# Performance work log

Measured on AMD Instinct MI355X. Metric: run time of the kernel, lower is better.

Reference implementation:

```python
import jax, jax.numpy as jnp
import numpy as np

N = 8192
IN_F = 512
OUT_F = 128
ALPHA = 0.2  # leaky relu negative slope
NEG_BIG = -1e10
RND_SCALE = 1e5


def setup_inputs() -> dict:
    key = jax.random.key(0)
    k1, k2, k3, k4, k5 = jax.random.split(key, 5)
    h = jax.random.normal(k1, (N, IN_F), dtype=jnp.float32)
    adj = jax.random.randint(k2, (N, N), 0, 2, dtype=jnp.int32)
    W = jax.random.normal(k3, (IN_F, OUT_F), dtype=jnp.float32) * 0.05
    a = jax.random.normal(k4, (2 * OUT_F, 1), dtype=jnp.float32) * 0.1
    # rnd in original is 1e5*(rand-0.5); same distribution here
    rnd = RND_SCALE * (jax.random.uniform(k5, (N, OUT_F), dtype=jnp.float32) - 0.5)
    return {"h": h, "adj": adj, "W": W, "a": a, "rnd": rnd}


def reference(h, adj, W, a, rnd):
    Wh = h @ W                              # [N, OUT_F]
    Wh1 = Wh @ a[:OUT_F, :]                 # [N, 1]
    Wh2 = Wh @ a[OUT_F:, :]                 # [N, 1]
    e = jax.nn.leaky_relu(Wh1 + Wh2.T, negative_slope=ALPHA)  # [N, N]
    attention = jnp.where(adj > 0, e, NEG_BIG)
    attention = jax.nn.softmax(attention, axis=1)
    h_prime = attention @ Wh                # [N, OUT_F]
    h_prime = (h_prime + rnd) / RND_SCALE
    return jax.nn.elu(h_prime)
```

## Files before the change

### kernel.cpp

```cpp
#include <hip/hip_runtime.h>

#define N 8192
#define IN_F 512
#define OUT_F 128
#define SPLITK 8
#define KC 1024
#define LOG2E 1.4426950408889634f
#define LN2 0.6931471805599453f

typedef __attribute__((ext_vector_type(4))) float f32x4;
typedef __attribute__((ext_vector_type(8))) short bf16x8;
typedef __attribute__((ext_vector_type(8))) unsigned short u16x8;
typedef __attribute__((ext_vector_type(4))) int i32x4;

__device__ __forceinline__ short f2bf(float f) {
    union { float f; unsigned u; } c; c.f = f;
    unsigned r = c.u + 0x7FFFu + ((c.u >> 16) & 1u);
    return (short)(r >> 16);
}

__device__ __forceinline__ float exp2fast(float x) {
#if __has_builtin(__builtin_amdgcn_exp2f)
    return __builtin_amdgcn_exp2f(x);
#else
    return __expf(x * LN2);
#endif
}

__device__ __forceinline__ void load_lds16(const void* g, void* l) {
    __builtin_amdgcn_global_load_lds((const __attribute__((address_space(1))) unsigned*)g,
                                     (__attribute__((address_space(3))) unsigned*)l,
                                     16, 0, 0);
}

__global__ __launch_bounds__(256) void prep(const float* __restrict__ W,
                                            short* __restrict__ WT) {
    int idx = blockIdx.x * 256 + threadIdx.x;
    int n = idx & (OUT_F - 1);
    int k = idx >> 7;
    WT[(size_t)n * IN_F + k] = f2bf(W[idx]);
}

__global__ __launch_bounds__(256) void gemm_hW(const float* __restrict__ h,
                                               const short* __restrict__ WT,
                                               const float* __restrict__ a,
                                               short* __restrict__ WhT,
                                               float* __restrict__ sOut,
                                               float* __restrict__ tOut) {
    const int tid = threadIdx.x;
    const int wave = tid >> 6, lane = tid & 63;
    const int row16 = lane & 15, kgrp = lane >> 4;
    const int m0 = blockIdx.x * 16;
    const int kbase = wave * 128;

    f32x4 acc[8] = {};
    const float4* hp = (const float4*)(h + (size_t)(m0 + row16) * IN_F + kbase);

#pragma unroll
    for (int kk = 0; kk < 128; kk += 32) {
        float4 u0 = hp[kk / 4 + kgrp * 2];
        float4 u1 = hp[kk / 4 + kgrp * 2 + 1];
        bf16x8 af;
        af[0] = f2bf(u0.x); af[1] = f2bf(u0.y); af[2] = f2bf(u0.z); af[3] = f2bf(u0.w);
        af[4] = f2bf(u1.x); af[5] = f2bf(u1.y); af[6] = f2bf(u1.z); af[7] = f2bf(u1.w);
#pragma unroll
        for (int nt = 0; nt < 8; nt++) {
            bf16x8 bf_ = *(const bf16x8*)(WT + (size_t)(nt * 16 + row16) * IN_F + kbase + kk + kgrp * 8);
            acc[nt] = __builtin_amdgcn_mfma_f32_16x16x32_bf16(af, bf_, acc[nt], 0, 0, 0);
        }
    }

    __shared__ float red[4][16][132];
#pragma unroll
    for (int nt = 0; nt < 8; nt++)
#pragma unroll
        for (int r = 0; r < 4; r++)
            red[wave][kgrp * 4 + r][nt * 16 + row16] = acc[nt][r];
    __syncthreads();

    const int row = tid >> 4, seg = tid & 15;
    float v[8];
#pragma unroll
    for (int e = 0; e < 8; e++) {
        int c = seg * 8 + e;
        v[e] = red[0][row][c] + red[1][row][c] + red[2][row][c] + red[3][row][c];
    }
    float sp = 0.f, tp = 0.f;
#pragma unroll
    for (int e = 0; e < 8; e++) {
        sp += v[e] * a[seg * 8 + e];
        tp += v[e] * a[OUT_F + seg * 8 + e];
    }
    sp += __shfl_xor(sp, 1); tp += __shfl_xor(tp, 1);
    sp += __shfl_xor(sp, 2); tp += __shfl_xor(tp, 2);
    sp += __shfl_xor(sp, 4); tp += __shfl_xor(tp, 4);
    sp += __shfl_xor(sp, 8); tp += __shfl_xor(tp, 8);
    if (seg == 0) {
        sOut[m0 + row] = sp * LOG2E;
        tOut[m0 + row] = tp * LOG2E;
    }
#pragma unroll
    for (int e = 0; e < 8; e++)
        WhT[(size_t)(seg * 8 + e) * N + m0 + row] = f2bf(v[e]);
}

__global__ __launch_bounds__(256, 4) void attn(const int* __restrict__ adj,
                                               const short* __restrict__ WhT,
                                               const float* __restrict__ s,
                                               const float* __restrict__ t,
                                               unsigned short* __restrict__ num,
                                               float* __restrict__ lpart) {
    const int tid = threadIdx.x;
    const int wave = tid >> 6, lane = tid & 63;
    const int row16 = lane & 15, kgrp = lane >> 4;
    const int kb = blockIdx.x & 7;
    const int mb = blockIdx.x >> 3;
    const int m0 = mb * 64 + wave * 16;
    const int m  = m0 + row16;
    const int ks = kb * KC;

    __shared__ short Bs[2][2][128 * 32];
    __shared__ float tl[KC];

    const i32x4* ap = (const i32x4*)(adj + (size_t)m * N + ks);
    const int abase = kgrp * 2;

    i32x4 ab[2][4];
#pragma unroll
    for (int d = 0; d < 2; d++)
#pragma unroll
        for (int hh = 0; hh < 2; hh++) {
            ab[0][d * 2 + hh] = __builtin_nontemporal_load(ap + d * 8 + abase + hh);
            ab[1][d * 2 + hh] = __builtin_nontemporal_load(ap + 16 + d * 8 + abase + hh);
        }

    for (int i = tid; i < KC; i += 256) tl[i] = t[ks + i];
    const float s_m = s[m];

    auto stageB = [&](int sup, int par) {
        const int k0 = ks + sup * 64;
#pragma unroll
        for (int d = 0; d < 2; d++)
#pragma unroll
            for (int q = 0; q < 2; q++) {
                int nrow = wave * 32 + q * 16 + (lane >> 2);
                const short* g = WhT + (size_t)nrow * N + k0 + d * 32 + (lane & 3) * 8;
                load_lds16(g, &Bs[par][d][(wave * 32 + q * 16) * 32]);
            }
    };

    f32x4 acc[8] = {};
    float lsum = 0.f;

    stageB(0, 0);
    __syncthreads();

    for (int spo = 0; spo < 8; spo++) {
#pragma unroll
        for (int ss = 0; ss < 2; ss++) {
            const int sp = spo * 2 + ss;
            const int par = ss;
            if (sp + 1 < 16) {
                stageB(sp + 1, par ^ 1);
                __builtin_amdgcn_sched_barrier(0);
            }
#pragma unroll
            for (int d = 0; d < 2; d++) {
                const int g = sp * 2 + d;
                const i32x4 a0 = ab[ss][d * 2 + 0];
                const i32x4 a1 = ab[ss][d * 2 + 1];

                const float* tp = tl + g * 32 + kgrp * 8;
                float4 tA = *(const float4*)tp;
                float4 tB = *(const float4*)(tp + 4);
                float tv[8] = { tA.x, tA.y, tA.z, tA.w, tB.x, tB.y, tB.z, tB.w };

                bf16x8 bfr[8];
                const short* base = &Bs[par][d][0];
#pragma unroll
                for (int ni = 0; ni < 8; ni++)
                    bfr[ni] = *(const bf16x8*)(base + (ni * 16 + row16) * 32 + kgrp * 8);

                bf16x8 af;
                unsigned* au = (unsigned*)&af;
#pragma unroll
                for (int q = 0; q < 4; q++) {
                    const int e0 = 2 * q, e1 = 2 * q + 1;
                    float x0 = s_m + tv[e0];
                    float x1 = s_m + tv[e1];
                    x0 = fmaxf(x0, 0.2f * x0);
                    x1 = fmaxf(x1, 0.2f * x1);
                    unsigned u0 = __float_as_uint(exp2fast(x0)) & 0xFFFF0000u;
                    unsigned u1 = __float_as_uint(exp2fast(x1)) & 0xFFFF0000u;
                    const int av0 = (e0 < 4) ? a0[e0] : a1[e0 - 4];
                    const int av1 = (e1 < 4) ? a0[e1] : a1[e1 - 4];
                    u0 = av0 > 0 ? u0 : 0u;
                    u1 = av1 > 0 ? u1 : 0u;
                    lsum += __uint_as_float(u0);
                    lsum += __uint_as_float(u1);
                    au[q] = (u0 >> 16) | u1;
                }

                if (d == 1 && sp + 2 < 16) {
                    __builtin_amdgcn_sched_barrier(0);
#pragma unroll
                    for (int dd = 0; dd < 2; dd++)
#pragma unroll
                        for (int hh = 0; hh < 2; hh++)
                            ab[ss][dd * 2 + hh] =
                                __builtin_nontemporal_load(ap + (sp + 2) * 16 + dd * 8 + abase + hh);
                    __builtin_amdgcn_sched_barrier(0);
                }

#pragma unroll
                for (int ni = 0; ni < 8; ni++)
                    acc[ni] = __builtin_amdgcn_mfma_f32_16x16x32_bf16(af, bfr[ni], acc[ni], 0, 0, 0);
            }
            asm volatile("s_waitcnt vmcnt(4)\n\ts_barrier" ::: "memory");
        }
    }

    {
        float v = lsum;
        v += __shfl_xor(v, 16);
        v += __shfl_xor(v, 32);
        if (kgrp == 0) lpart[(size_t)kb * N + m] = v;
    }

    unsigned short* np_ = num + ((size_t)kb * N + m0) * OUT_F;
#pragma unroll
    for (int ni = 0; ni < 8; ni++) {
        int n = ni * 16 + row16;
#pragma unroll
        for (int r = 0; r < 4; r++)
            np_[(size_t)(kgrp * 4 + r) * OUT_F + n] = (unsigned short)f2bf(acc[ni][r]);
    }
}

__global__ __launch_bounds__(256) void finalize(const unsigned short* __restrict__ num,
                                                const float* __restrict__ lpart,
                                                const float* __restrict__ rnd,
                                                float* __restrict__ out) {
    int idx = blockIdx.x * 256 + threadIdx.x;
    int m = idx >> 4;
    int c = (idx & 15) * 8;
    size_t g = (size_t)m * OUT_F + c;

    float nm[8] = {};
#pragma unroll
    for (int bk = 0; bk < SPLITK; bk++) {
        u16x8 v = *(const u16x8*)(num + (size_t)bk * N * OUT_F + g);
#pragma unroll
        for (int e = 0; e < 8; e++) nm[e] += __uint_as_float((unsigned)v[e] << 16);
    }
    float l = 0.f;
#pragma unroll
    for (int bk = 0; bk < SPLITK; bk++) l += lpart[(size_t)bk * N + m];
    float inv = 1.f / fmaxf(l, 1e-30f);

    float4 r0 = *(const float4*)(rnd + g);
    float4 r1 = *(const float4*)(rnd + g + 4);
    float rv[8] = { r0.x, r0.y, r0.z, r0.w, r1.x, r1.y, r1.z, r1.w };
    float ov[8];
#pragma unroll
    for (int e = 0; e < 8; e++) {
        float x = (nm[e] * inv + rv[e]) * 1e-5f;
        ov[e] = x > 0.f ? x : __expf(x) - 1.f;
    }
    *(float4*)(out + g)     = make_float4(ov[0], ov[1], ov[2], ov[3]);
    *(float4*)(out + g + 4) = make_float4(ov[4], ov[5], ov[6], ov[7]);
}

extern "C" void kernel_launch(void* const* d_in, const int* in_sizes, int n_in,
                              void* d_out, int out_size, void* d_ws, size_t ws_size,
                              hipStream_t stream) {
    const float* h   = (const float*)d_in[0];
    const int*   adj = (const int*)d_in[1];
    const float* W   = (const float*)d_in[2];
    const float* a   = (const float*)d_in[3];
    const float* rnd = (const float*)d_in[4];
    float* out = (float*)d_out;

    char* w = (char*)d_ws;
    short* WT    = (short*)(w);
    short* WhT   = (short*)(w + 131072);
    float* sv    = (float*)(w + 2228224);
    float* tv    = (float*)(w + 2260992);
    float* lpart = (float*)(w + 2293760);
    unsigned short* num  = (unsigned short*)(w + 2555904);

    prep    <<<256, 256, 0, stream>>>(W, WT);
    gemm_hW <<<512, 256, 0, stream>>>(h, WT, a, WhT, sv, tv);
    attn    <<<1024, 256, 0, stream>>>(adj, WhT, sv, tv, num, lpart);
    finalize<<<512, 256, 0, stream>>>(num, lpart, rnd, out);
}
```

Before: 416.2 us.

## Load WhT B-fragments and t directly from global, dropping LDS staging and barriers

Removes the LDS double-buffered staging of WhT tiles and the t vector in the attention kernel. Each wave now reads its bf16 B fragments and t values straight from global memory (relying on L2/cache reuse across waves), which eliminates the per-step s_barrier and waitcnt synchronisation. Launch bounds occupancy hint drops from 4 to 3 blocks per SIMD to allow more registers for the in-flight global loads. This trades redundant global/L2 traffic (each of the four waves re-reads the same B tile) for less synchronisation and LDS use.

Result: slower. 504.9 us (+21.3%).

```diff
diff --git a/kernel.cpp b/kernel.cpp
--- a/kernel.cpp
+++ b/kernel.cpp
@@ -25,12 +25,6 @@
 #else
     return __expf(x * LN2);
 #endif
-}
-
-__device__ __forceinline__ void load_lds16(const void* g, void* l) {
-    __builtin_amdgcn_global_load_lds((const __attribute__((address_space(1))) unsigned*)g,
-                                     (__attribute__((address_space(3))) unsigned*)l,
-                                     16, 0, 0);
 }
 
 __global__ __launch_bounds__(256) void prep(const float* __restrict__ W,
@@ -104,7 +98,7 @@
         WhT[(size_t)(seg * 8 + e) * N + m0 + row] = f2bf(v[e]);
 }
 
-__global__ __launch_bounds__(256, 4) void attn(const int* __restrict__ adj,
+__global__ __launch_bounds__(256, 3) void attn(const int* __restrict__ adj,
                                                const short* __restrict__ WhT,
                                                const float* __restrict__ s,
                                                const float* __restrict__ t,
@@ -119,9 +113,6 @@
     const int m  = m0 + row16;
     const int ks = kb * KC;
 
-    __shared__ short Bs[2][2][128 * 32];
-    __shared__ float tl[KC];
-
     const i32x4* ap = (const i32x4*)(adj + (size_t)m * N + ks);
     const int abase = kgrp * 2;
 
@@ -134,89 +125,64 @@
             ab[1][d * 2 + hh] = __builtin_nontemporal_load(ap + 16 + d * 8 + abase + hh);
         }
 
-    for (int i = tid; i < KC; i += 256) tl[i] = t[ks + i];
     const float s_m = s[m];
-
-    auto stageB = [&](int sup, int par) {
-        const int k0 = ks + sup * 64;
-#pragma unroll
-        for (int d = 0; d < 2; d++)
-#pragma unroll
-            for (int q = 0; q < 2; q++) {
-                int nrow = wave * 32 + q * 16 + (lane >> 2);
-                const short* g = WhT + (size_t)nrow * N + k0 + d * 32 + (lane & 3) * 8;
-                load_lds16(g, &Bs[par][d][(wave * 32 + q * 16) * 32]);
-            }
-    };
 
     f32x4 acc[8] = {};
     float lsum = 0.f;
 
-    stageB(0, 0);
-    __syncthreads();
-
-    for (int spo = 0; spo < 8; spo++) {
-#pragma unroll
-        for (int ss = 0; ss < 2; ss++) {
-            const int sp = spo * 2 + ss;
-            const int par = ss;
-            if (sp + 1 < 16) {
-                stageB(sp + 1, par ^ 1);
+    for (int sp = 0; sp < 16; sp++) {
+        const int ss = sp & 1;
+        const int k0 = ks + sp * 64;
+#pragma unroll
+        for (int d = 0; d < 2; d++) {
+            const int g = sp * 2 + d;
+            const i32x4 a0 = ab[ss][d * 2 + 0];
+            const i32x4 a1 = ab[ss][d * 2 + 1];
+
+            bf16x8 bfr[8];
+            const short* bb = WhT + k0 + d * 32 + kgrp * 8 + (size_t)row16 * N;
+#pragma unroll
+            for (int ni = 0; ni < 8; ni++)
+                bfr[ni] = *(const bf16x8*)(bb + (size_t)(ni * 16) * N);
+
+            const float* tp = t + ks + g * 32 + kgrp * 8;
+            float4 tA = *(const float4*)tp;
+            float4 tB = *(const float4*)(tp + 4);
+            float tv[8] = { tA.x, tA.y, tA.z, tA.w, tB.x, tB.y, tB.z, tB.w };
+
+            if (d == 1 && sp + 2 < 16) {
+                __builtin_amdgcn_sched_barrier(0);
+#pragma unroll
+                for (int dd = 0; dd < 2; dd++)
+#pragma unroll
+                    for (int hh = 0; hh < 2; hh++)
+                        ab[ss][dd * 2 + hh] =
+                            __builtin_nontemporal_load(ap + (sp + 2) * 16 + dd * 8 + abase + hh);
                 __builtin_amdgcn_sched_barrier(0);
             }
-#pragma unroll
-            for (int d = 0; d < 2; d++) {
-                const int g = sp * 2 + d;
-                const i32x4 a0 = ab[ss][d * 2 + 0];
-                const i32x4 a1 = ab[ss][d * 2 + 1];
-
-                const float* tp = tl + g * 32 + kgrp * 8;
-                float4 tA = *(const float4*)tp;
-                float4 tB = *(const float4*)(tp + 4);
-                float tv[8] = { tA.x, tA.y, tA.z, tA.w, tB.x, tB.y, tB.z, tB.w };
-
-                bf16x8 bfr[8];
-                const short* base = &Bs[par][d][0];
-#pragma unroll
-                for (int ni = 0; ni < 8; ni++)
-                    bfr[ni] = *(const bf16x8*)(base + (ni * 16 + row16) * 32 + kgrp * 8);
-
-                bf16x8 af;
-                unsigned* au = (unsigned*)&af;
-#pragma unroll
-                for (int q = 0; q < 4; q++) {
-                    const int e0 = 2 * q, e1 = 2 * q + 1;
-                    float x0 = s_m + tv[e0];
-                    float x1 = s_m + tv[e1];
-                    x0 = fmaxf(x0, 0.2f * x0);
-                    x1 = fmaxf(x1, 0.2f * x1);
-                    unsigned u0 = __float_as_uint(exp2fast(x0)) & 0xFFFF0000u;
-                    unsigned u1 = __float_as_uint(exp2fast(x1)) & 0xFFFF0000u;
-                    const int av0 = (e0 < 4) ? a0[e0] : a1[e0 - 4];
-                    const int av1 = (e1 < 4) ? a0[e1] : a1[e1 - 4];
-                    u0 = av0 > 0 ? u0 : 0u;
-                    u1 = av1 > 0 ? u1 : 0u;
-                    lsum += __uint_as_float(u0);
-                    lsum += __uint_as_float(u1);
-                    au[q] = (u0 >> 16) | u1;
-                }
-
-                if (d == 1 && sp + 2 < 16) {
-                    __builtin_amdgcn_sched_barrier(0);
-#pragma unroll
-                    for (int dd = 0; dd < 2; dd++)
-#pragma unroll
-                        for (int hh = 0; hh < 2; hh++)
-                            ab[ss][dd * 2 + hh] =
-                                __builtin_nontemporal_load(ap + (sp + 2) * 16 + dd * 8 + abase + hh);
-                    __builtin_amdgcn_sched_barrier(0);
-                }
-
-#pragma unroll
-                for (int ni = 0; ni < 8; ni++)
-                    acc[ni] = __builtin_amdgcn_mfma_f32_16x16x32_bf16(af, bfr[ni], acc[ni], 0, 0, 0);
+
+            bf16x8 af;
+            unsigned* au = (unsigned*)&af;
+#pragma unroll
+            for (int q = 0; q < 4; q++) {
+                const int e0 = 2 * q, e1 = 2 * q + 1;
+                float x0 = s_m + tv[e0];
+                float x1 = s_m + tv[e1];
+                x0 = fmaxf(x0, 0.2f * x0);
+                x1 = fmaxf(x1, 0.2f * x1);
+                unsigned u0 = __float_as_uint(exp2fast(x0)) & 0xFFFF0000u;
+                unsigned u1 = __float_as_uint(exp2fast(x1)) & 0xFFFF0000u;
+                const int av0 = (e0 < 4) ? a0[e0] : a1[e0 - 4];
+                const int av1 = (e1 < 4) ? a0[e1] : a1[e1 - 4];
+                u0 = av0 > 0 ? u0 : 0u;
+                u1 = av1 > 0 ? u1 : 0u;
+                lsum += __uint_as_float(u0);
+                lsum += __uint_as_float(u1);
+                au[q] = (u0 >> 16) | u1;
             }
-            asm volatile("s_waitcnt vmcnt(4)\n\ts_barrier" ::: "memory");
+#pragma unroll
+            for (int ni = 0; ni < 8; ni++)
+                acc[ni] = __builtin_amdgcn_mfma_f32_16x16x32_bf16(af, bfr[ni], acc[ni], 0, 0, 0);
         }
     }
 
```
